# Kernel optimization log

Measured on AMD Instinct MI355X. Metric: run time of the kernel, lower is better.

## Reference

```python
import jax, jax.numpy as jnp
from jax import lax
import numpy as np

NPOINT = 1024
NSAMPLE = 32
RADIUS = 0.1
BN_EPS = 1e-5


def setup_inputs() -> dict:
    key = jax.random.key(0)
    k1, k2, k3 = jax.random.split(key, 3)
    B, N, C = 8, 4096, 128
    C_in, C_out = C + 3, 256
    xyz = jax.random.uniform(k1, (B, N, 3), dtype=jnp.float32)
    features = jax.random.normal(k2, (B, N, C), dtype=jnp.float32)
    W = jax.random.normal(k3, (C_out, C_in), dtype=jnp.float32) * 0.05
    b = jnp.zeros((C_out,), jnp.float32)
    return {
        "xyz": xyz,
        "features": features,
        "W": W,
        "b": b,
        "bn_gamma": jnp.ones((C_in,), jnp.float32),
        "bn_beta": jnp.zeros((C_in,), jnp.float32),
        "bn_mean": jnp.zeros((C_in,), jnp.float32),
        "bn_var": jnp.ones((C_in,), jnp.float32),
    }


def furthest_point_sample(xyz, npoint):
    # xyz: (B, N, 3) -> idx (B, npoint) int32; matches CUDA kernel (starts at index 0)
    B, N, _ = xyz.shape

    def step(carry, _):
        mind, last = carry  # (B,N), (B,)
        p = jnp.take_along_axis(xyz, last[:, None, None], axis=1)  # (B,1,3)
        d = jnp.sum((xyz - p) ** 2, axis=-1)  # (B,N)
        mind = jnp.minimum(mind, d)
        nxt = jnp.argmax(mind, axis=-1).astype(jnp.int32)
        return (mind, nxt), nxt

    init = (jnp.full((B, N), 1e10, xyz.dtype), jnp.zeros((B,), jnp.int32))
    _, rest = lax.scan(step, init, None, length=npoint - 1)  # (npoint-1, B)
    idx = jnp.concatenate([jnp.zeros((1, B), jnp.int32), rest], axis=0)
    return idx.T  # (B, npoint)


def ball_query(xyz, new_xyz, radius, nsample):
    # first `nsample` points of xyz within radius of each new_xyz, padded with first hit
    B, N, _ = xyz.shape
    d2 = jnp.sum((new_xyz[:, :, None, :] - xyz[:, None, :, :]) ** 2, axis=-1)  # (B,S,N)
    valid = d2 < radius * radius
    score = jnp.where(valid, jnp.arange(N, dtype=jnp.int32), jnp.int32(N))  # (B,S,N)
    neg_vals, _ = lax.top_k(-score, nsample)  # smallest indices first
    idx = -neg_vals  # (B,S,K)
    first = idx[..., :1]  # centroid is always within radius of itself
    idx = jnp.where(idx >= N, first, idx)
    return idx


def reference(xyz, features, W, b, bn_gamma, bn_beta, bn_mean, bn_var):
    B = xyz.shape[0]
    fps_idx = furthest_point_sample(xyz, NPOINT)  # (B,S)
    new_xyz = jnp.take_along_axis(xyz, fps_idx[:, :, None], axis=1)  # (B,S,3)
    idx = ball_query(xyz, new_xyz, RADIUS, NSAMPLE)  # (B,S,K)
    bidx = jnp.arange(B)[:, None, None]
    g_xyz = xyz[bidx, idx] - new_xyz[:, :, None, :]  # (B,S,K,3) centered
    g_feat = features[bidx, idx]  # (B,S,K,C)
    x = jnp.concatenate([g_xyz, g_feat], axis=-1)  # (B,S,K,C+3) use_xyz=True
    # PointConv: BN (eval) -> ReLU -> 1x1 conv -> max over nsample
    x = (x - bn_mean) * (bn_gamma / jnp.sqrt(bn_var + BN_EPS)) + bn_beta
    x = jax.nn.relu(x)
    y = jnp.einsum('bskc,oc->bsko', x, W) + b  # (B,S,K,O)
    y = jnp.max(y, axis=2)  # (B,S,O)
    new_features = jnp.transpose(y, (0, 2, 1))  # (B,O,S) like torch layout
    return new_xyz, new_features
```

## Files before the change

### kernel.cpp

```cpp
#pragma clang fp contract(off)
#include <hip/hip_runtime.h>
#include <math.h>

#define N_PTS   4096
#define B_SZ    8
#define NPOINT  1024
#define NSAMPLE 32
#define C_FEAT  128
#define C_IN    131
#define C_OUT   256
#define R2      1e-2f

#define KT      5
#define NT      16
#define KPAD    168

typedef __attribute__((ext_vector_type(8))) short bf16x8;
typedef __attribute__((ext_vector_type(4))) float f32x4;
typedef __attribute__((ext_vector_type(2))) float v2f;

__device__ __forceinline__ unsigned short f2bf(float f) {
    unsigned u = __float_as_uint(f);
    return (unsigned short)((u + 0x7FFF + ((u >> 16) & 1)) >> 16);
}
__device__ __forceinline__ float bf2f(unsigned short h) {
    return __uint_as_float(((unsigned)h) << 16);
}

__device__ __forceinline__ v2f pk_add(v2f a, v2f b) {
    v2f d; asm("v_pk_add_f32 %0, %1, %2" : "=v"(d) : "v"(a), "v"(b)); return d;
}
__device__ __forceinline__ v2f pk_mul(v2f a, v2f b) {
    v2f d; asm("v_pk_mul_f32 %0, %1, %2" : "=v"(d) : "v"(a), "v"(b)); return d;
}

__global__ __launch_bounds__(64) void k_wtrans(const float* __restrict__ W,
                                               unsigned short* __restrict__ Wb_hi,
                                               unsigned short* __restrict__ Wb_lo) {
    const int blk  = blockIdx.x;
    const int kt   = blk / NT, nt = blk % NT;
    const int lane = threadIdx.x;
    const int o    = nt * 16 + (lane & 15);
    const int k0   = kt * 32 + (lane >> 4) * 8;
    const size_t base = ((size_t)blk * 64 + lane) * 8;
#pragma unroll
    for (int j = 0; j < 8; ++j) {
        int k = k0 + j;
        float v = 0.0f;
        if (k < C_IN) {
            int src = (k < C_FEAT) ? (k + 3) : (k - C_FEAT);
            v = W[o * C_IN + src];
        }
        unsigned short hh = f2bf(v);
        Wb_hi[base + j] = hh;
        Wb_lo[base + j] = f2bf(v - bf2f(hh));
    }
}

#define FPS_BLOCK 256
#define FPS_PPT   16
#define FPS_NW    (FPS_BLOCK / 64)

#define DPP_ARGMAX(vb, vi, ctrl, rmask)                                           \
    do {                                                                          \
        int _nb = __builtin_amdgcn_update_dpp(vb, vb, ctrl, rmask, 0xf, false);   \
        int _ni = __builtin_amdgcn_update_dpp(vi, vi, ctrl, rmask, 0xf, false);   \
        bool _g = (_nb >= vb);                                                    \
        vb = _g ? _nb : vb;                                                       \
        vi = _g ? _ni : vi;                                                       \
    } while (0)

#define CMB(ab, aj, bb_, bj_)                                                     \
    do {                                                                          \
        bool _g = ((bb_) > (ab));                                                 \
        ab = _g ? (bb_) : (ab);                                                   \
        aj = _g ? (bj_) : (aj);                                                   \
    } while (0)

__global__ __launch_bounds__(FPS_BLOCK) void k_fps(const float* __restrict__ xyz,
                                                   float* __restrict__ new_xyz) {
    const int b    = blockIdx.x;
    const int t    = threadIdx.x;
    const int lane = t & 63;
    const int wid  = t >> 6;
    __shared__ float4 xyzw[N_PTS];
    __shared__ unsigned long long red[2][FPS_NW];

    const float* base = xyz + (size_t)b * N_PTS * 3;

    v2f nX[8], nY[8], nZ[8], M[8];

    const float4* b4 = (const float4*)(base + (size_t)t * (FPS_PPT * 3));
    float4 v[12];
#pragma unroll
    for (int i = 0; i < 12; ++i) v[i] = b4[i];
    const float* vf = (const float*)v;
#pragma unroll
    for (int p = 0; p < 8; ++p) {
        float x0 = vf[(2 * p) * 3 + 0], x1 = vf[(2 * p + 1) * 3 + 0];
        float y0 = vf[(2 * p) * 3 + 1], y1 = vf[(2 * p + 1) * 3 + 1];
        float z0 = vf[(2 * p) * 3 + 2], z1 = vf[(2 * p + 1) * 3 + 2];
        nX[p] = (v2f){-x0, -x1};
        nY[p] = (v2f){-y0, -y1};
        nZ[p] = (v2f){-z0, -z1};
        M[p]  = (v2f){1e10f, 1e10f};
        int gi = t * FPS_PPT + 2 * p;
        xyzw[gi]     = (float4){x0, y0, z0, 0.0f};
        xyzw[gi + 1] = (float4){x1, y1, z1, 0.0f};
    }
    __syncthreads();

    float4 c4 = xyzw[0];
    float cx = c4.x, cy = c4.y, cz = c4.z;
    if (t == 0) {
        float* o = new_xyz + (size_t)b * NPOINT * 3;
        o[0] = cx; o[1] = cy; o[2] = cz;
    }

    for (int it = 1; it < NPOINT; ++it) {
        const v2f ccx = (v2f){cx, cx};
        const v2f ccy = (v2f){cy, cy};
        const v2f ccz = (v2f){cz, cz};
        int pb[8], pj[8];
#pragma unroll
        for (int p = 0; p < 8; ++p) {
            v2f dx = pk_add(nX[p], ccx);
            v2f dy = pk_add(nY[p], ccy);
            v2f dz = pk_add(nZ[p], ccz);
            v2f xx = pk_mul(dx, dx);
            v2f yy = pk_mul(dy, dy);
            v2f zz = pk_mul(dz, dz);
            v2f d  = pk_add(pk_add(xx, yy), zz);
            M[p].x = fminf(M[p].x, d.x);
            M[p].y = fminf(M[p].y, d.y);
            int bx = __float_as_int(M[p].x);
            int by = __float_as_int(M[p].y);
            bool g = by > bx;
            pb[p] = g ? by : bx;
            pj[p] = g ? (2 * p + 1) : (2 * p);
        }
        CMB(pb[0], pj[0], pb[1], pj[1]);
        CMB(pb[2], pj[2], pb[3], pj[3]);
        CMB(pb[4], pj[4], pb[5], pj[5]);
        CMB(pb[6], pj[6], pb[7], pj[7]);
        CMB(pb[0], pj[0], pb[2], pj[2]);
        CMB(pb[4], pj[4], pb[6], pj[6]);
        CMB(pb[0], pj[0], pb[4], pj[4]);
        int vb = pb[0];
        int vi = t * FPS_PPT + pj[0];
        DPP_ARGMAX(vb, vi, 0x111, 0xf);
        DPP_ARGMAX(vb, vi, 0x112, 0xf);
        DPP_ARGMAX(vb, vi, 0x114, 0xf);
        DPP_ARGMAX(vb, vi, 0x118, 0xf);
        DPP_ARGMAX(vb, vi, 0x142, 0xa);
        DPP_ARGMAX(vb, vi, 0x143, 0xc);
        if (lane == 63)
            red[it & 1][wid] = ((unsigned long long)(unsigned)vb << 32)
                             | (unsigned)(N_PTS - 1 - vi);
        __syncthreads();
        const unsigned long long* rp = red[it & 1];
        unsigned long long k0 = rp[0], k1 = rp[1], k2 = rp[2], k3 = rp[3];
        unsigned long long b01 = k0 > k1 ? k0 : k1;
        unsigned long long b23 = k2 > k3 ? k2 : k3;
        unsigned long long best = b01 > b23 ? b01 : b23;
        const int idx = N_PTS - 1 - (int)(best & 0xFFFFull);
        float4 w4 = xyzw[idx];
        cx = w4.x; cy = w4.y; cz = w4.z;
        if (t == 0) {
            float* o = new_xyz + ((size_t)b * NPOINT + it) * 3;
            o[0] = cx; o[1] = cy; o[2] = cz;
        }
    }
}

__global__ __launch_bounds__(256) void k_ballquery(const float* __restrict__ xyz,
                                                   const float* __restrict__ new_xyz,
                                                   int* __restrict__ out_idx) {
    const int lane = threadIdx.x & 63;
    const int wid  = threadIdx.x >> 6;
    const int b    = blockIdx.y;
    const int s    = blockIdx.x * 4 + wid;

    const float* xb = xyz + (size_t)b * N_PTS * 3;
    const float* q  = new_xyz + ((size_t)b * NPOINT + s) * 3;
    float qx = q[0], qy = q[1], qz = q[2];
    int* ob = out_idx + ((size_t)b * NPOINT + s) * NSAMPLE;

    int total = 0, first = -1;
    const unsigned long long mlt = (1ull << lane) - 1ull;

    for (int ch = 0; ch < N_PTS / 64; ++ch) {
        int i = ch * 64 + lane;
        float x = xb[i * 3 + 0], y = xb[i * 3 + 1], z = xb[i * 3 + 2];
        float dx = qx - x, dy = qy - y, dz = qz - z;
        float d2 = ((dx * dx) + (dy * dy)) + (dz * dz);
        bool valid = d2 < R2;
        unsigned long long m = __ballot(valid);
        if (valid) {
            int pos = total + __popcll(m & mlt);
            if (pos < NSAMPLE) ob[pos] = i;
        }
        if (first < 0 && m != 0ull) first = ch * 64 + (__ffsll(m) - 1);
        total += __popcll(m);
        if (total >= NSAMPLE) break;
    }
    if (total < NSAMPLE) {
        if (lane >= total && lane < NSAMPLE) ob[lane] = first;
    }
}

__device__ __forceinline__ float bn_relu(float v, float mean, float scale, float beta) {
    float r = ((v - mean) * scale) + beta;
    return fmaxf(r, 0.0f);
}

__global__ __launch_bounds__(256) void k_group_gemm(
    const float* __restrict__ xyz, const float* __restrict__ feat,
    const float* __restrict__ new_xyz, const int* __restrict__ idx,
    const unsigned short* __restrict__ Wb_hi, const unsigned short* __restrict__ Wb_lo,
    const float* __restrict__ bias,
    const float* __restrict__ bn_g, const float* __restrict__ bn_b,
    const float* __restrict__ bn_m, const float* __restrict__ bn_v,
    float* __restrict__ out) {
    const int sx = blockIdx.x;
    const int s  = ((sx & 7) << 7) | (sx >> 3);
    const int b  = blockIdx.y;
    const int t  = threadIdx.x;
    const int lane = t & 63;
    const int w    = t >> 6;

    __shared__ unsigned short Xh[32][KPAD], Xl[32][KPAD];
    __shared__ float sc_l[C_IN], mn_l[C_IN], bt_l[C_IN];
    __shared__ int   idxs[NSAMPLE];
    __shared__ float nq[3];

    if (t < C_IN) {
        float g  = bn_g[t];
        float vv = bn_v[t] + 1e-5f;
        sc_l[t] = g / sqrtf(vv);
        mn_l[t] = bn_m[t];
        bt_l[t] = bn_b[t];
    }
    if (t < NSAMPLE) idxs[t] = idx[((size_t)b * NPOINT + s) * NSAMPLE + t];
    if (t < 3)       nq[t]   = new_xyz[((size_t)b * NPOINT + s) * 3 + t];
    __syncthreads();

    {
        const int ks = t & 31;
        const int qh = t >> 5;
        const float* frow = feat + ((size_t)b * N_PTS + idxs[ks]) * C_FEAT;
#pragma unroll
        for (int m = 0; m < 4; ++m) {
            int qq = m * 8 + qh;
            int c0 = qq * 4;
            float4 f = *(const float4*)&frow[c0];
            float v0 = bn_relu(f.x, mn_l[3 + c0 + 0], sc_l[3 + c0 + 0], bt_l[3 + c0 + 0]);
            float v1 = bn_relu(f.y, mn_l[3 + c0 + 1], sc_l[3 + c0 + 1], bt_l[3 + c0 + 1]);
            float v2 = bn_relu(f.z, mn_l[3 + c0 + 2], sc_l[3 + c0 + 2], bt_l[3 + c0 + 2]);
            float v3 = bn_relu(f.w, mn_l[3 + c0 + 3], sc_l[3 + c0 + 3], bt_l[3 + c0 + 3]);
            unsigned short h0 = f2bf(v0), h1 = f2bf(v1), h2 = f2bf(v2), h3 = f2bf(v3);
            uint2 hv, lv;
            hv.x = (unsigned)h0 | ((unsigned)h1 << 16);
            hv.y = (unsigned)h2 | ((unsigned)h3 << 16);
            lv.x = (unsigned)f2bf(v0 - bf2f(h0)) | ((unsigned)f2bf(v1 - bf2f(h1)) << 16);
            lv.y = (unsigned)f2bf(v2 - bf2f(h2)) | ((unsigned)f2bf(v3 - bf2f(h3)) << 16);
            *(uint2*)&Xh[ks][c0] = hv;
            *(uint2*)&Xl[ks][c0] = lv;
        }
    }
    if (t < 32) {
        const int row = t;
        const int id  = idxs[row];
        const float* p = xyz + ((size_t)b * N_PTS + id) * 3;
        uint4 z4 = {0u, 0u, 0u, 0u};
        uint4 hh = z4, ll = z4;
        unsigned short h[3];
#pragma unroll
        for (int d = 0; d < 3; ++d) {
            float g = p[d] - nq[d];
            float v = bn_relu(g, mn_l[d], sc_l[d], bt_l[d]);
            h[d] = f2bf(v);
            unsigned short lo = f2bf(v - bf2f(h[d]));
            if (d == 0) { hh.x |= h[d];                 ll.x |= lo; }
            if (d == 1) { hh.x |= (unsigned)h[d] << 16; ll.x |= (unsigned)lo << 16; }
            if (d == 2) { hh.y |= h[d];                 ll.y |= lo; }
        }
        *(uint4*)&Xh[row][128] = hh;  *(uint4*)&Xl[row][128] = ll;
        *(uint4*)&Xh[row][136] = z4;  *(uint4*)&Xl[row][136] = z4;
        *(uint4*)&Xh[row][144] = z4;  *(uint4*)&Xl[row][144] = z4;
        *(uint4*)&Xh[row][152] = z4;  *(uint4*)&Xl[row][152] = z4;
        *(uint4*)&Xh[row][160] = z4;  *(uint4*)&Xl[row][160] = z4;
    }
    __syncthreads();

    f32x4 zero = {0.f, 0.f, 0.f, 0.f};
    f32x4 acc[2][4];
#pragma unroll
    for (int m = 0; m < 2; ++m)
#pragma unroll
        for (int n = 0; n < 4; ++n) acc[m][n] = zero;

    const int r0 = lane & 15;
#pragma unroll
    for (int kt = 0; kt < KT; ++kt) {
        const int k0 = kt * 32 + (lane >> 4) * 8;
        bf16x8 a0h = *(const bf16x8*)&Xh[r0][k0];
        bf16x8 a1h = *(const bf16x8*)&Xh[16 + r0][k0];
        bf16x8 a0l = *(const bf16x8*)&Xl[r0][k0];
        bf16x8 a1l = *(const bf16x8*)&Xl[16 + r0][k0];
#pragma unroll
        for (int n = 0; n < 4; ++n) {
            const int nt = w * 4 + n;
            const size_t off = (((size_t)kt * NT + nt) * 64 + lane) * 8;
            bf16x8 bh = *(const bf16x8*)&Wb_hi[off];
            bf16x8 bl = *(const bf16x8*)&Wb_lo[off];
            acc[0][n] = __builtin_amdgcn_mfma_f32_16x16x32_bf16(a0h, bh, acc[0][n], 0, 0, 0);
            acc[1][n] = __builtin_amdgcn_mfma_f32_16x16x32_bf16(a1h, bh, acc[1][n], 0, 0, 0);
            acc[0][n] = __builtin_amdgcn_mfma_f32_16x16x32_bf16(a0l, bh, acc[0][n], 0, 0, 0);
            acc[1][n] = __builtin_amdgcn_mfma_f32_16x16x32_bf16(a1l, bh, acc[1][n], 0, 0, 0);
            acc[0][n] = __builtin_amdgcn_mfma_f32_16x16x32_bf16(a0h, bl, acc[0][n], 0, 0, 0);
            acc[1][n] = __builtin_amdgcn_mfma_f32_16x16x32_bf16(a1h, bl, acc[1][n], 0, 0, 0);
        }
    }

#pragma unroll
    for (int n = 0; n < 4; ++n) {
        float m0 = fmaxf(acc[0][n][0], acc[1][n][0]);
        float m1 = fmaxf(acc[0][n][1], acc[1][n][1]);
        float m2 = fmaxf(acc[0][n][2], acc[1][n][2]);
        float m3 = fmaxf(acc[0][n][3], acc[1][n][3]);
        float pm = fmaxf(fmaxf(m0, m1), fmaxf(m2, m3));
        pm = fmaxf(pm, __shfl_xor(pm, 16));
        pm = fmaxf(pm, __shfl_xor(pm, 32));
        if (lane < 16) {
            int o = (w * 4 + n) * 16 + lane;
            out[(size_t)b * C_OUT * NPOINT + (size_t)o * NPOINT + s] = pm + bias[o];
        }
    }
}

extern "C" void kernel_launch(void* const* d_in, const int* in_sizes, int n_in,
                              void* d_out, int out_size, void* d_ws, size_t ws_size,
                              hipStream_t stream) {
    const float* xyz  = (const float*)d_in[0];
    const float* feat = (const float*)d_in[1];
    const float* W    = (const float*)d_in[2];
    const float* bias = (const float*)d_in[3];
    const float* bn_g = (const float*)d_in[4];
    const float* bn_b = (const float*)d_in[5];
    const float* bn_m = (const float*)d_in[6];
    const float* bn_v = (const float*)d_in[7];

    float* new_xyz  = (float*)d_out;
    float* out_feat = (float*)d_out + (size_t)B_SZ * NPOINT * 3;

    int*            ws_idx = (int*)d_ws;
    unsigned short* Wb_hi  = (unsigned short*)((char*)d_ws + (size_t)B_SZ * NPOINT * NSAMPLE * sizeof(int));
    unsigned short* Wb_lo  = Wb_hi + (size_t)KT * NT * 64 * 8;

    hipLaunchKernelGGL(k_wtrans, dim3(KT * NT), dim3(64), 0, stream, W, Wb_hi, Wb_lo);
    hipLaunchKernelGGL(k_fps, dim3(B_SZ), dim3(FPS_BLOCK), 0, stream, xyz, new_xyz);
    hipLaunchKernelGGL(k_ballquery, dim3(NPOINT / 4, B_SZ), dim3(256), 0, stream,
                       xyz, new_xyz, ws_idx);
    hipLaunchKernelGGL(k_group_gemm, dim3(NPOINT, B_SZ), dim3(256), 0, stream,
                       xyz, feat, new_xyz, ws_idx, Wb_hi, Wb_lo, bias,
                       bn_g, bn_b, bn_m, bn_v, out_feat);
}
```

Before: 807.0 us.

## Fuse FPS, ball query and grouped GEMM into one persistent kernel with progress flags

Replaces the three separate kernels with one persistent kernel of 256 blocks. The first 8 blocks run furthest point sampling and publish progress per batch through atomic counters. All blocks then pull work items from an atomic queue, spin until the needed centroid is ready, and do the ball query and the bf16-split MFMA GEMM in-block. This lets the grouping and GEMM overlap with the serial FPS and drops the index buffer round trip. In exchange, the FPS blocks share compute units with worker blocks, the design relies on co-residency and spin-waits, and the large shared-memory footprint lowers occupancy.

```diff
diff --git a/kernel.cpp b/kernel.cpp
--- a/kernel.cpp
+++ b/kernel.cpp
@@ -14,6 +14,7 @@
 #define KT      5
 #define NT      16
 #define KPAD    168
+#define NITEMS  (B_SZ * NPOINT)
 
 typedef __attribute__((ext_vector_type(8))) short bf16x8;
 typedef __attribute__((ext_vector_type(4))) float f32x4;
@@ -32,6 +33,10 @@
 }
 __device__ __forceinline__ v2f pk_mul(v2f a, v2f b) {
     v2f d; asm("v_pk_mul_f32 %0, %1, %2" : "=v"(d) : "v"(a), "v"(b)); return d;
+}
+
+__global__ void k_zero(unsigned* __restrict__ ctrl) {
+    if (threadIdx.x < 16) ctrl[threadIdx.x] = 0u;
 }
 
 __global__ __launch_bounds__(64) void k_wtrans(const float* __restrict__ W,
@@ -61,10 +66,10 @@
 #define FPS_PPT   16
 #define FPS_NW    (FPS_BLOCK / 64)
 
-#define DPP_ARGMAX(vb, vi, ctrl, rmask)                                           \
+#define DPP_ARGMAX(vb, vi, ctrl_, rmask)                                          \
     do {                                                                          \
-        int _nb = __builtin_amdgcn_update_dpp(vb, vb, ctrl, rmask, 0xf, false);   \
-        int _ni = __builtin_amdgcn_update_dpp(vi, vi, ctrl, rmask, 0xf, false);   \
+        int _nb = __builtin_amdgcn_update_dpp(vb, vb, ctrl_, rmask, 0xf, false);  \
+        int _ni = __builtin_amdgcn_update_dpp(vi, vi, ctrl_, rmask, 0xf, false);  \
         bool _g = (_nb >= vb);                                                    \
         vb = _g ? _nb : vb;                                                       \
         vi = _g ? _ni : vi;                                                       \
@@ -77,162 +82,129 @@
         aj = _g ? (bj_) : (aj);                                                   \
     } while (0)
 
-__global__ __launch_bounds__(FPS_BLOCK) void k_fps(const float* __restrict__ xyz,
-                                                   float* __restrict__ new_xyz) {
-    const int b    = blockIdx.x;
-    const int t    = threadIdx.x;
-    const int lane = t & 63;
-    const int wid  = t >> 6;
-    __shared__ float4 xyzw[N_PTS];
-    __shared__ unsigned long long red[2][FPS_NW];
-
-    const float* base = xyz + (size_t)b * N_PTS * 3;
-
-    v2f nX[8], nY[8], nZ[8], M[8];
-
-    const float4* b4 = (const float4*)(base + (size_t)t * (FPS_PPT * 3));
-    float4 v[12];
-#pragma unroll
-    for (int i = 0; i < 12; ++i) v[i] = b4[i];
-    const float* vf = (const float*)v;
-#pragma unroll
-    for (int p = 0; p < 8; ++p) {
-        float x0 = vf[(2 * p) * 3 + 0], x1 = vf[(2 * p + 1) * 3 + 0];
-        float y0 = vf[(2 * p) * 3 + 1], y1 = vf[(2 * p + 1) * 3 + 1];
-        float z0 = vf[(2 * p) * 3 + 2], z1 = vf[(2 * p + 1) * 3 + 2];
-        nX[p] = (v2f){-x0, -x1};
-        nY[p] = (v2f){-y0, -y1};
-        nZ[p] = (v2f){-z0, -z1};
-        M[p]  = (v2f){1e10f, 1e10f};
-        int gi = t * FPS_PPT + 2 * p;
-        xyzw[gi]     = (float4){x0, y0, z0, 0.0f};
-        xyzw[gi + 1] = (float4){x1, y1, z1, 0.0f};
-    }
-    __syncthreads();
-
-    float4 c4 = xyzw[0];
-    float cx = c4.x, cy = c4.y, cz = c4.z;
-    if (t == 0) {
-        float* o = new_xyz + (size_t)b * NPOINT * 3;
-        o[0] = cx; o[1] = cy; o[2] = cz;
-    }
-
-    for (int it = 1; it < NPOINT; ++it) {
-        const v2f ccx = (v2f){cx, cx};
-        const v2f ccy = (v2f){cy, cy};
-        const v2f ccz = (v2f){cz, cz};
-        int pb[8], pj[8];
-#pragma unroll
-        for (int p = 0; p < 8; ++p) {
-            v2f dx = pk_add(nX[p], ccx);
-            v2f dy = pk_add(nY[p], ccy);
-            v2f dz = pk_add(nZ[p], ccz);
-            v2f xx = pk_mul(dx, dx);
-            v2f yy = pk_mul(dy, dy);
-            v2f zz = pk_mul(dz, dz);
-            v2f d  = pk_add(pk_add(xx, yy), zz);
-            M[p].x = fminf(M[p].x, d.x);
-            M[p].y = fminf(M[p].y, d.y);
-            int bx = __float_as_int(M[p].x);
-            int by = __float_as_int(M[p].y);
-            bool g = by > bx;
-            pb[p] = g ? by : bx;
-            pj[p] = g ? (2 * p + 1) : (2 * p);
-        }
-        CMB(pb[0], pj[0], pb[1], pj[1]);
-        CMB(pb[2], pj[2], pb[3], pj[3]);
-        CMB(pb[4], pj[4], pb[5], pj[5]);
-        CMB(pb[6], pj[6], pb[7], pj[7]);
-        CMB(pb[0], pj[0], pb[2], pj[2]);
-        CMB(pb[4], pj[4], pb[6], pj[6]);
-        CMB(pb[0], pj[0], pb[4], pj[4]);
-        int vb = pb[0];
-        int vi = t * FPS_PPT + pj[0];
-        DPP_ARGMAX(vb, vi, 0x111, 0xf);
-        DPP_ARGMAX(vb, vi, 0x112, 0xf);
-        DPP_ARGMAX(vb, vi, 0x114, 0xf);
-        DPP_ARGMAX(vb, vi, 0x118, 0xf);
-        DPP_ARGMAX(vb, vi, 0x142, 0xa);
-        DPP_ARGMAX(vb, vi, 0x143, 0xc);
-        if (lane == 63)
-            red[it & 1][wid] = ((unsigned long long)(unsigned)vb << 32)
-                             | (unsigned)(N_PTS - 1 - vi);
-        __syncthreads();
-        const unsigned long long* rp = red[it & 1];
-        unsigned long long k0 = rp[0], k1 = rp[1], k2 = rp[2], k3 = rp[3];
-        unsigned long long b01 = k0 > k1 ? k0 : k1;
-        unsigned long long b23 = k2 > k3 ? k2 : k3;
-        unsigned long long best = b01 > b23 ? b01 : b23;
-        const int idx = N_PTS - 1 - (int)(best & 0xFFFFull);
-        float4 w4 = xyzw[idx];
-        cx = w4.x; cy = w4.y; cz = w4.z;
-        if (t == 0) {
-            float* o = new_xyz + ((size_t)b * NPOINT + it) * 3;
-            o[0] = cx; o[1] = cy; o[2] = cz;
-        }
-    }
-}
-
-__global__ __launch_bounds__(256) void k_ballquery(const float* __restrict__ xyz,
-                                                   const float* __restrict__ new_xyz,
-                                                   int* __restrict__ out_idx) {
-    const int lane = threadIdx.x & 63;
-    const int wid  = threadIdx.x >> 6;
-    const int b    = blockIdx.y;
-    const int s    = blockIdx.x * 4 + wid;
-
-    const float* xb = xyz + (size_t)b * N_PTS * 3;
-    const float* q  = new_xyz + ((size_t)b * NPOINT + s) * 3;
-    float qx = q[0], qy = q[1], qz = q[2];
-    int* ob = out_idx + ((size_t)b * NPOINT + s) * NSAMPLE;
-
-    int total = 0, first = -1;
-    const unsigned long long mlt = (1ull << lane) - 1ull;
-
-    for (int ch = 0; ch < N_PTS / 64; ++ch) {
-        int i = ch * 64 + lane;
-        float x = xb[i * 3 + 0], y = xb[i * 3 + 1], z = xb[i * 3 + 2];
-        float dx = qx - x, dy = qy - y, dz = qz - z;
-        float d2 = ((dx * dx) + (dy * dy)) + (dz * dz);
-        bool valid = d2 < R2;
-        unsigned long long m = __ballot(valid);
-        if (valid) {
-            int pos = total + __popcll(m & mlt);
-            if (pos < NSAMPLE) ob[pos] = i;
-        }
-        if (first < 0 && m != 0ull) first = ch * 64 + (__ffsll(m) - 1);
-        total += __popcll(m);
-        if (total >= NSAMPLE) break;
-    }
-    if (total < NSAMPLE) {
-        if (lane >= total && lane < NSAMPLE) ob[lane] = first;
-    }
-}
-
 __device__ __forceinline__ float bn_relu(float v, float mean, float scale, float beta) {
     float r = ((v - mean) * scale) + beta;
     return fmaxf(r, 0.0f);
 }
 
-__global__ __launch_bounds__(256) void k_group_gemm(
+__global__ __launch_bounds__(256) void k_mega(
     const float* __restrict__ xyz, const float* __restrict__ feat,
-    const float* __restrict__ new_xyz, const int* __restrict__ idx,
     const unsigned short* __restrict__ Wb_hi, const unsigned short* __restrict__ Wb_lo,
     const float* __restrict__ bias,
     const float* __restrict__ bn_g, const float* __restrict__ bn_b,
     const float* __restrict__ bn_m, const float* __restrict__ bn_v,
-    float* __restrict__ out) {
-    const int sx = blockIdx.x;
-    const int s  = ((sx & 7) << 7) | (sx >> 3);
-    const int b  = blockIdx.y;
-    const int t  = threadIdx.x;
+    float* new_xyz, float* __restrict__ out, unsigned* ctrl) {
+    __shared__ char smem[84000];
+    const int t    = threadIdx.x;
     const int lane = t & 63;
-    const int w    = t >> 6;
-
-    __shared__ unsigned short Xh[32][KPAD], Xl[32][KPAD];
-    __shared__ float sc_l[C_IN], mn_l[C_IN], bt_l[C_IN];
-    __shared__ int   idxs[NSAMPLE];
-    __shared__ float nq[3];
+    const int wid  = t >> 6;
+
+    if (blockIdx.x < B_SZ) {
+        float4* xyzw = (float4*)smem;
+        unsigned long long (*red)[FPS_NW] = (unsigned long long (*)[FPS_NW])(smem + 65536);
+        const int b = blockIdx.x;
+        const float* base = xyz + (size_t)b * N_PTS * 3;
+
+        v2f nX[8], nY[8], nZ[8], M[8];
+        const float4* b4 = (const float4*)(base + (size_t)t * (FPS_PPT * 3));
+        float4 v[12];
+#pragma unroll
+        for (int i = 0; i < 12; ++i) v[i] = b4[i];
+        const float* vf = (const float*)v;
+#pragma unroll
+        for (int p = 0; p < 8; ++p) {
+            float x0 = vf[(2 * p) * 3 + 0], x1 = vf[(2 * p + 1) * 3 + 0];
+            float y0 = vf[(2 * p) * 3 + 1], y1 = vf[(2 * p + 1) * 3 + 1];
+            float z0 = vf[(2 * p) * 3 + 2], z1 = vf[(2 * p + 1) * 3 + 2];
+            nX[p] = (v2f){-x0, -x1};
+            nY[p] = (v2f){-y0, -y1};
+            nZ[p] = (v2f){-z0, -z1};
+            M[p]  = (v2f){1e10f, 1e10f};
+            int gi = t * FPS_PPT + 2 * p;
+            xyzw[gi]     = (float4){x0, y0, z0, 0.0f};
+            xyzw[gi + 1] = (float4){x1, y1, z1, 0.0f};
+        }
+        __syncthreads();
+
+        float4 c4 = xyzw[0];
+        float cx = c4.x, cy = c4.y, cz = c4.z;
+        if (t == 0) {
+            float* o = new_xyz + (size_t)b * NPOINT * 3;
+            __hip_atomic_store(&o[0], cx, __ATOMIC_RELAXED, __HIP_MEMORY_SCOPE_AGENT);
+            __hip_atomic_store(&o[1], cy, __ATOMIC_RELAXED, __HIP_MEMORY_SCOPE_AGENT);
+            __hip_atomic_store(&o[2], cz, __ATOMIC_RELAXED, __HIP_MEMORY_SCOPE_AGENT);
+        }
+
+        for (int it = 1; it < NPOINT; ++it) {
+            const v2f ccx = (v2f){cx, cx};
+            const v2f ccy = (v2f){cy, cy};
+            const v2f ccz = (v2f){cz, cz};
+            int pb[8], pj[8];
+#pragma unroll
+            for (int p = 0; p < 8; ++p) {
+                v2f dx = pk_add(nX[p], ccx);
+                v2f dy = pk_add(nY[p], ccy);
+                v2f dz = pk_add(nZ[p], ccz);
+                v2f xx = pk_mul(dx, dx);
+                v2f yy = pk_mul(dy, dy);
+                v2f zz = pk_mul(dz, dz);
+                v2f d  = pk_add(pk_add(xx, yy), zz);
+                M[p].x = fminf(M[p].x, d.x);
+                M[p].y = fminf(M[p].y, d.y);
+                int bx = __float_as_int(M[p].x);
+                int by = __float_as_int(M[p].y);
+                bool g = by > bx;
+                pb[p] = g ? by : bx;
+                pj[p] = g ? (2 * p + 1) : (2 * p);
+            }
+            CMB(pb[0], pj[0], pb[1], pj[1]);
+            CMB(pb[2], pj[2], pb[3], pj[3]);
+            CMB(pb[4], pj[4], pb[5], pj[5]);
+            CMB(pb[6], pj[6], pb[7], pj[7]);
+            CMB(pb[0], pj[0], pb[2], pj[2]);
+            CMB(pb[4], pj[4], pb[6], pj[6]);
+            CMB(pb[0], pj[0], pb[4], pj[4]);
+            int vb = pb[0];
+            int vi = t * FPS_PPT + pj[0];
+            DPP_ARGMAX(vb, vi, 0x111, 0xf);
+            DPP_ARGMAX(vb, vi, 0x112, 0xf);
+            DPP_ARGMAX(vb, vi, 0x114, 0xf);
+            DPP_ARGMAX(vb, vi, 0x118, 0xf);
+            DPP_ARGMAX(vb, vi, 0x142, 0xa);
+            DPP_ARGMAX(vb, vi, 0x143, 0xc);
+            if (lane == 63)
+                red[it & 1][wid] = ((unsigned long long)(unsigned)vb << 32)
+                                 | (unsigned)(N_PTS - 1 - vi);
+            __syncthreads();
+            const unsigned long long* rp = red[it & 1];
+            unsigned long long k0 = rp[0], k1 = rp[1], k2 = rp[2], k3 = rp[3];
+            unsigned long long b01 = k0 > k1 ? k0 : k1;
+            unsigned long long b23 = k2 > k3 ? k2 : k3;
+            unsigned long long best = b01 > b23 ? b01 : b23;
+            const int idx = N_PTS - 1 - (int)(best & 0xFFFFull);
+            float4 w4 = xyzw[idx];
+            cx = w4.x; cy = w4.y; cz = w4.z;
+            if (t == 0) {
+                float* o = new_xyz + ((size_t)b * NPOINT + it) * 3;
+                __hip_atomic_store(&o[0], cx, __ATOMIC_RELAXED, __HIP_MEMORY_SCOPE_AGENT);
+                __hip_atomic_store(&o[1], cy, __ATOMIC_RELAXED, __HIP_MEMORY_SCOPE_AGENT);
+                __hip_atomic_store(&o[2], cz, __ATOMIC_RELAXED, __HIP_MEMORY_SCOPE_AGENT);
+                if ((it & 15) == 15)
+                    __hip_atomic_store(&ctrl[b], (unsigned)(it + 1),
+                                       __ATOMIC_RELEASE, __HIP_MEMORY_SCOPE_AGENT);
+            }
+        }
+        __syncthreads();
+    }
+
+    unsigned short (*Xh)[KPAD] = (unsigned short (*)[KPAD])smem;
+    unsigned short (*Xl)[KPAD] = (unsigned short (*)[KPAD])(smem + 10752);
+    float* sc_l = (float*)(smem + 21504);
+    float* mn_l = (float*)(smem + 22032);
+    float* bt_l = (float*)(smem + 22560);
+    int*   idxs = (int*)(smem + 23088);
+    float* nq   = (float*)(smem + 23216);
+    int*   itsl = (int*)(smem + 23232);
 
     if (t < C_IN) {
         float g  = bn_g[t];
@@ -241,100 +213,143 @@
         mn_l[t] = bn_m[t];
         bt_l[t] = bn_b[t];
     }
-    if (t < NSAMPLE) idxs[t] = idx[((size_t)b * NPOINT + s) * NSAMPLE + t];
-    if (t < 3)       nq[t]   = new_xyz[((size_t)b * NPOINT + s) * 3 + t];
     __syncthreads();
 
-    {
-        const int ks = t & 31;
-        const int qh = t >> 5;
-        const float* frow = feat + ((size_t)b * N_PTS + idxs[ks]) * C_FEAT;
-#pragma unroll
-        for (int m = 0; m < 4; ++m) {
-            int qq = m * 8 + qh;
-            int c0 = qq * 4;
-            float4 f = *(const float4*)&frow[c0];
-            float v0 = bn_relu(f.x, mn_l[3 + c0 + 0], sc_l[3 + c0 + 0], bt_l[3 + c0 + 0]);
-            float v1 = bn_relu(f.y, mn_l[3 + c0 + 1], sc_l[3 + c0 + 1], bt_l[3 + c0 + 1]);
-            float v2 = bn_relu(f.z, mn_l[3 + c0 + 2], sc_l[3 + c0 + 2], bt_l[3 + c0 + 2]);
-            float v3 = bn_relu(f.w, mn_l[3 + c0 + 3], sc_l[3 + c0 + 3], bt_l[3 + c0 + 3]);
-            unsigned short h0 = f2bf(v0), h1 = f2bf(v1), h2 = f2bf(v2), h3 = f2bf(v3);
-            uint2 hv, lv;
-            hv.x = (unsigned)h0 | ((unsigned)h1 << 16);
-            hv.y = (unsigned)h2 | ((unsigned)h3 << 16);
-            lv.x = (unsigned)f2bf(v0 - bf2f(h0)) | ((unsigned)f2bf(v1 - bf2f(h1)) << 16);
-            lv.y = (unsigned)f2bf(v2 - bf2f(h2)) | ((unsigned)f2bf(v3 - bf2f(h3)) << 16);
-            *(uint2*)&Xh[ks][c0] = hv;
-            *(uint2*)&Xl[ks][c0] = lv;
-        }
-    }
-    if (t < 32) {
-        const int row = t;
-        const int id  = idxs[row];
-        const float* p = xyz + ((size_t)b * N_PTS + id) * 3;
-        uint4 z4 = {0u, 0u, 0u, 0u};
-        uint4 hh = z4, ll = z4;
-        unsigned short h[3];
-#pragma unroll
-        for (int d = 0; d < 3; ++d) {
-            float g = p[d] - nq[d];
-            float v = bn_relu(g, mn_l[d], sc_l[d], bt_l[d]);
-            h[d] = f2bf(v);
-            unsigned short lo = f2bf(v - bf2f(h[d]));
-            if (d == 0) { hh.x |= h[d];                 ll.x |= lo; }
-            if (d == 1) { hh.x |= (unsigned)h[d] << 16; ll.x |= (unsigned)lo << 16; }
-            if (d == 2) { hh.y |= h[d];                 ll.y |= lo; }
-        }
-        *(uint4*)&Xh[row][128] = hh;  *(uint4*)&Xl[row][128] = ll;
-        *(uint4*)&Xh[row][136] = z4;  *(uint4*)&Xl[row][136] = z4;
-        *(uint4*)&Xh[row][144] = z4;  *(uint4*)&Xl[row][144] = z4;
-        *(uint4*)&Xh[row][152] = z4;  *(uint4*)&Xl[row][152] = z4;
-        *(uint4*)&Xh[row][160] = z4;  *(uint4*)&Xl[row][160] = z4;
-    }
-    __syncthreads();
-
-    f32x4 zero = {0.f, 0.f, 0.f, 0.f};
-    f32x4 acc[2][4];
-#pragma unroll
-    for (int m = 0; m < 2; ++m)
-#pragma unroll
-        for (int n = 0; n < 4; ++n) acc[m][n] = zero;
-
-    const int r0 = lane & 15;
-#pragma unroll
-    for (int kt = 0; kt < KT; ++kt) {
-        const int k0 = kt * 32 + (lane >> 4) * 8;
-        bf16x8 a0h = *(const bf16x8*)&Xh[r0][k0];
-        bf16x8 a1h = *(const bf16x8*)&Xh[16 + r0][k0];
-        bf16x8 a0l = *(const bf16x8*)&Xl[r0][k0];
-        bf16x8 a1l = *(const bf16x8*)&Xl[16 + r0][k0];
+    for (;;) {
+        if (t == 0) *itsl = (int)atomicAdd(&ctrl[8], 1u);
+        __syncthreads();
+        const int item = *itsl;
+        if (item >= NITEMS) break;
+        const int s  = item >> 3;
+        const int bb = item & 7;
+        if (t == 0) {
+            while ((int)__hip_atomic_load(&ctrl[bb], __ATOMIC_RELAXED,
+                                          __HIP_MEMORY_SCOPE_AGENT) < s + 1)
+                __builtin_amdgcn_s_sleep(16);
+        }
+        __syncthreads();
+
+        if (wid == 0) {
+            float* qp = new_xyz + ((size_t)bb * NPOINT + s) * 3;
+            float qx = __hip_atomic_load(&qp[0], __ATOMIC_RELAXED, __HIP_MEMORY_SCOPE_AGENT);
+            float qy = __hip_atomic_load(&qp[1], __ATOMIC_RELAXED, __HIP_MEMORY_SCOPE_AGENT);
+            float qz = __hip_atomic_load(&qp[2], __ATOMIC_RELAXED, __HIP_MEMORY_SCOPE_AGENT);
+            if (lane == 0) { nq[0] = qx; nq[1] = qy; nq[2] = qz; }
+            const float* xb = xyz + (size_t)bb * N_PTS * 3;
+            int total = 0, first = -1;
+            const unsigned long long mlt = (1ull << lane) - 1ull;
+            for (int ch = 0; ch < N_PTS / 64; ++ch) {
+                int i2 = ch * 64 + lane;
+                float x = xb[i2 * 3 + 0], y = xb[i2 * 3 + 1], z = xb[i2 * 3 + 2];
+                float dx = qx - x, dy = qy - y, dz = qz - z;
+                float d2 = ((dx * dx) + (dy * dy)) + (dz * dz);
+                bool valid = d2 < R2;
+                unsigned long long m = __ballot(valid);
+                if (valid) {
+                    int pos = total + __popcll(m & mlt);
+                    if (pos < NSAMPLE) idxs[pos] = i2;
+                }
+                if (first < 0 && m != 0ull) first = ch * 64 + (__ffsll(m) - 1);
+                total += __popcll(m);
+                if (total >= NSAMPLE) break;
+            }
+            if (total < NSAMPLE) {
+                if (lane >= total && lane < NSAMPLE) idxs[lane] = first;
+            }
+        }
+        __syncthreads();
+
+        {
+            const int ks = t & 31;
+            const int qh = t >> 5;
+            const float* frow = feat + ((size_t)bb * N_PTS + idxs[ks]) * C_FEAT;
+#pragma unroll
+            for (int m2 = 0; m2 < 4; ++m2) {
+                int qq = m2 * 8 + qh;
+                int c0 = qq * 4;
+                float4 f = *(const float4*)&frow[c0];
+                float v0 = bn_relu(f.x, mn_l[3 + c0 + 0], sc_l[3 + c0 + 0], bt_l[3 + c0 + 0]);
+                float v1 = bn_relu(f.y, mn_l[3 + c0 + 1], sc_l[3 + c0 + 1], bt_l[3 + c0 + 1]);
+                float v2 = bn_relu(f.z, mn_l[3 + c0 + 2], sc_l[3 + c0 + 2], bt_l[3 + c0 + 2]);
+                float v3 = bn_relu(f.w, mn_l[3 + c0 + 3], sc_l[3 + c0 + 3], bt_l[3 + c0 + 3]);
+                unsigned short h0 = f2bf(v0), h1 = f2bf(v1), h2 = f2bf(v2), h3 = f2bf(v3);
+                uint2 hv, lv;
+                hv.x = (unsigned)h0 | ((unsigned)h1 << 16);
+                hv.y = (unsigned)h2 | ((unsigned)h3 << 16);
+                lv.x = (unsigned)f2bf(v0 - bf2f(h0)) | ((unsigned)f2bf(v1 - bf2f(h1)) << 16);
+                lv.y = (unsigned)f2bf(v2 - bf2f(h2)) | ((unsigned)f2bf(v3 - bf2f(h3)) << 16);
+                *(uint2*)&Xh[ks][c0] = hv;
+                *(uint2*)&Xl[ks][c0] = lv;
+            }
+        }
+        if (t < 32) {
+            const int row = t;
+            const int id  = idxs[row];
+            const float* p = xyz + ((size_t)bb * N_PTS + id) * 3;
+            uint4 z4 = {0u, 0u, 0u, 0u};
+            uint4 hh = z4, ll = z4;
+            unsigned short h[3];
+#pragma unroll
+            for (int d = 0; d < 3; ++d) {
+                float g = p[d] - nq[d];
+                float vv = bn_relu(g, mn_l[d], sc_l[d], bt_l[d]);
+                h[d] = f2bf(vv);
+                unsigned short lo = f2bf(vv - bf2f(h[d]));
+                if (d == 0) { hh.x |= h[d];                 ll.x |= lo; }
+                if (d == 1) { hh.x |= (unsigned)h[d] << 16; ll.x |= (unsigned)lo << 16; }
+                if (d == 2) { hh.y |= h[d];                 ll.y |= lo; }
+            }
+            *(uint4*)&Xh[row][128] = hh;  *(uint4*)&Xl[row][128] = ll;
+            *(uint4*)&Xh[row][136] = z4;  *(uint4*)&Xl[row][136] = z4;
+            *(uint4*)&Xh[row][144] = z4;  *(uint4*)&Xl[row][144] = z4;
+            *(uint4*)&Xh[row][152] = z4;  *(uint4*)&Xl[row][152] = z4;
+            *(uint4*)&Xh[row][160] = z4;  *(uint4*)&Xl[row][160] = z4;
+        }
+        __syncthreads();
+
+        f32x4 zero = {0.f, 0.f, 0.f, 0.f};
+        f32x4 acc[2][4];
+#pragma unroll
+        for (int m2 = 0; m2 < 2; ++m2)
+#pragma unroll
+            for (int n = 0; n < 4; ++n) acc[m2][n] = zero;
+
+        const int r0 = lane & 15;
+#pragma unroll
+        for (int kt = 0; kt < KT; ++kt) {
+            const int k0 = kt * 32 + (lane >> 4) * 8;
+            bf16x8 a0h = *(const bf16x8*)&Xh[r0][k0];
+            bf16x8 a1h = *(const bf16x8*)&Xh[16 + r0][k0];
+            bf16x8 a0l = *(const bf16x8*)&Xl[r0][k0];
+            bf16x8 a1l = *(const bf16x8*)&Xl[16 + r0][k0];
+#pragma unroll
+            for (int n = 0; n < 4; ++n) {
+                const int nt = wid * 4 + n;
+                const size_t off = (((size_t)kt * NT + nt) * 64 + lane) * 8;
+                bf16x8 bh = *(const bf16x8*)&Wb_hi[off];
+                bf16x8 bl = *(const bf16x8*)&Wb_lo[off];
+                acc[0][n] = __builtin_amdgcn_mfma_f32_16x16x32_bf16(a0h, bh, acc[0][n], 0, 0, 0);
+                acc[1][n] = __builtin_amdgcn_mfma_f32_16x16x32_bf16(a1h, bh, acc[1][n], 0, 0, 0);
+                acc[0][n] = __builtin_amdgcn_mfma_f32_16x16x32_bf16(a0l, bh, acc[0][n], 0, 0, 0);
+                acc[1][n] = __builtin_amdgcn_mfma_f32_16x16x32_bf16(a1l, bh, acc[1][n], 0, 0, 0);
+                acc[0][n] = __builtin_amdgcn_mfma_f32_16x16x32_bf16(a0h, bl, acc[0][n], 0, 0, 0);
+                acc[1][n] = __builtin_amdgcn_mfma_f32_16x16x32_bf16(a1h, bl, acc[1][n], 0, 0, 0);
+            }
+        }
+
 #pragma unroll
         for (int n = 0; n < 4; ++n) {
-            const int nt = w * 4 + n;
-            const size_t off = (((size_t)kt * NT + nt) * 64 + lane) * 8;
-            bf16x8 bh = *(const bf16x8*)&Wb_hi[off];
-            bf16x8 bl = *(const bf16x8*)&Wb_lo[off];
-            acc[0][n] = __builtin_amdgcn_mfma_f32_16x16x32_bf16(a0h, bh, acc[0][n], 0, 0, 0);
-            acc[1][n] = __builtin_amdgcn_mfma_f32_16x16x32_bf16(a1h, bh, acc[1][n], 0, 0, 0);
-            acc[0][n] = __builtin_amdgcn_mfma_f32_16x16x32_bf16(a0l, bh, acc[0][n], 0, 0, 0);
-            acc[1][n] = __builtin_amdgcn_mfma_f32_16x16x32_bf16(a1l, bh, acc[1][n], 0, 0, 0);
-            acc[0][n] = __builtin_amdgcn_mfma_f32_16x16x32_bf16(a0h, bl, acc[0][n], 0, 0, 0);
-            acc[1][n] = __builtin_amdgcn_mfma_f32_16x16x32_bf16(a1h, bl, acc[1][n], 0, 0, 0);
-        }
-    }
-
-#pragma unroll
-    for (int n = 0; n < 4; ++n) {
-        float m0 = fmaxf(acc[0][n][0], acc[1][n][0]);
-        float m1 = fmaxf(acc[0][n][1], acc[1][n][1]);
-        float m2 = fmaxf(acc[0][n][2], acc[1][n][2]);
-        float m3 = fmaxf(acc[0][n][3], acc[1][n][3]);
-        float pm = fmaxf(fmaxf(m0, m1), fmaxf(m2, m3));
-        pm = fmaxf(pm, __shfl_xor(pm, 16));
-        pm = fmaxf(pm, __shfl_xor(pm, 32));
-        if (lane < 16) {
-            int o = (w * 4 + n) * 16 + lane;
-            out[(size_t)b * C_OUT * NPOINT + (size_t)o * NPOINT + s] = pm + bias[o];
+            float m0 = fmaxf(acc[0][n][0], acc[1][n][0]);
+            float m1 = fmaxf(acc[0][n][1], acc[1][n][1]);
+            float m2 = fmaxf(acc[0][n][2], acc[1][n][2]);
+            float m3 = fmaxf(acc[0][n][3], acc[1][n][3]);
+            float pm = fmaxf(fmaxf(m0, m1), fmaxf(m2, m3));
+            pm = fmaxf(pm, __shfl_xor(pm, 16));
+            pm = fmaxf(pm, __shfl_xor(pm, 32));
+            if (lane < 16) {
+                int o = (wid * 4 + n) * 16 + lane;
+                out[(size_t)bb * C_OUT * NPOINT + (size_t)o * NPOINT + s] = pm + bias[o];
+            }
         }
     }
 }
@@ -354,15 +369,13 @@
     float* new_xyz  = (float*)d_out;
     float* out_feat = (float*)d_out + (size_t)B_SZ * NPOINT * 3;
 
-    int*            ws_idx = (int*)d_ws;
-    unsigned short* Wb_hi  = (unsigned short*)((char*)d_ws + (size_t)B_SZ * NPOINT * NSAMPLE * sizeof(int));
-    unsigned short* Wb_lo  = Wb_hi + (size_t)KT * NT * 64 * 8;
-
+    unsigned short* Wb_hi = (unsigned short*)d_ws;
+    unsigned short* Wb_lo = Wb_hi + (size_t)KT * NT * 64 * 8;
+    unsigned*       ctrl  = (unsigned*)((char*)d_ws + 163840);
+
+    hipLaunchKernelGGL(k_zero,   dim3(1),       dim3(64), 0, stream, ctrl);
     hipLaunchKernelGGL(k_wtrans, dim3(KT * NT), dim3(64), 0, stream, W, Wb_hi, Wb_lo);
-    hipLaunchKernelGGL(k_fps, dim3(B_SZ), dim3(FPS_BLOCK), 0, stream, xyz, new_xyz);
-    hipLaunchKernelGGL(k_ballquery, dim3(NPOINT / 4, B_SZ), dim3(256), 0, stream,
-                       xyz, new_xyz, ws_idx);
-    hipLaunchKernelGGL(k_group_gemm, dim3(NPOINT, B_SZ), dim3(256), 0, stream,
-                       xyz, feat, new_xyz, ws_idx, Wb_hi, Wb_lo, bias,
-                       bn_g, bn_b, bn_m, bn_v, out_feat);
-}
+    hipLaunchKernelGGL(k_mega,   dim3(256),     dim3(256), 0, stream,
+                       xyz, feat, Wb_hi, Wb_lo, bias,
+                       bn_g, bn_b, bn_m, bn_v, new_xyz, out_feat, ctrl);
+}
```

Result: faster. 772.4 us (-4.3%).
